# Kernel tuning notes

Hardware: AMD Instinct MI355X
Metric: run time of the kernel (lower is better)

The kernel has to match this reference:

```python
import jax, jax.numpy as jnp
import numpy as np

IN_CH, OUT_CH, SUPPORT = 128, 128, 3
BS, N = 8, 2048


def knn_idx(x, k):
    # x: (bs, n, d) -> (bs, n, k) indices of k nearest (excluding self)
    sq = jnp.sum(x * x, axis=-1)  # (bs, n)
    dist = sq[:, :, None] + sq[:, None, :] - 2.0 * jnp.einsum('bnd,bmd->bnm', x, x)
    _, idx = jax.lax.top_k(-dist, k + 1)  # smallest distances
    return idx[:, :, 1:]


def gather_neighbors(t, idx):
    # t: (bs, n, d), idx: (bs, n, k) -> (bs, n, k, d)
    return jax.vmap(lambda tb, ib: tb[ib])(t, idx)


def l2_normalize(x, axis, eps=1e-12):
    n = jnp.linalg.norm(x, axis=axis, keepdims=True)
    return x / jnp.maximum(n, eps)


def setup_inputs() -> dict:
    key = jax.random.key(0)
    ks = jax.random.split(key, 8)
    stdv = 1.0 / np.sqrt(OUT_CH * (SUPPORT + 1))
    return {
        'vertices': jax.random.normal(ks[0], (BS, N, 3), jnp.float32),
        'feature_map': jax.random.normal(ks[1], (BS, N, IN_CH), jnp.float32),
        'weights': jax.random.uniform(ks[2], (IN_CH, (SUPPORT + 1) * OUT_CH), jnp.float32, -stdv, stdv),
        'bias': jax.random.uniform(ks[3], ((SUPPORT + 1) * OUT_CH,), jnp.float32, -stdv, stdv),
        'directions': jax.random.uniform(ks[4], (3, SUPPORT * OUT_CH), jnp.float32, -stdv, stdv),
        'ste_w': jax.random.normal(ks[5], (OUT_CH, IN_CH), jnp.float32) * (1.0 / np.sqrt(IN_CH)),
        'conv2_w': jax.random.normal(ks[6], (OUT_CH, 2 * OUT_CH), jnp.float32) * (1.0 / np.sqrt(2 * OUT_CH)),
        'neighbor_num': 16,
    }


def reference(vertices, feature_map, weights, bias, directions, ste_w, conv2_w, neighbor_num):
    bs, n, _ = vertices.shape
    k = neighbor_num

    # STE branch: 1x1 conv == per-point linear
    f_ste = jnp.einsum('bnc,oc->bno', feature_map, ste_w)

    # Receptive fields: KNN in feature space ('RF-F'), directions from vertices
    neighbor_index = knn_idx(feature_map, k)                      # (bs, n, k)
    neighbors = gather_neighbors(vertices, neighbor_index)        # (bs, n, k, 3)
    rf_norm = l2_normalize(neighbors - vertices[:, :, None, :], axis=-1)

    # Graph convolution (3D-GCN style)
    sdn = l2_normalize(directions, axis=0)                        # (3, s*out)
    theta = jax.nn.relu(jnp.einsum('bnkd,dm->bnkm', rf_norm, sdn))  # (bs,n,k,s*out)
    fm = feature_map @ weights + bias                             # (bs,n,(s+1)*out)
    feature_center = fm[:, :, :OUT_CH]
    feature_support = gather_neighbors(fm[:, :, OUT_CH:], neighbor_index)  # (bs,n,k,s*out)
    act = (theta * feature_support).reshape(bs, n, k, SUPPORT, OUT_CH)
    act = jnp.max(act, axis=2)          # max over neighbors
    act = jnp.mean(act, axis=2)         # mean over supports
    feature = feature_center + act      # (bs, n, out)

    # ORL: global context via point-space KNN max-pool
    nb_idx2 = knn_idx(vertices, k)
    pooled = jnp.max(gather_neighbors(feature, nb_idx2), axis=2)  # (bs,n,out)
    f_global = jnp.broadcast_to(jnp.mean(pooled, axis=1, keepdims=True), (bs, n, OUT_CH))
    feat_cat = jnp.concatenate([feature, f_global], axis=-1)      # (bs,n,2*out)
    feature_fuse = jnp.einsum('bnc,oc->bno', feat_cat, conv2_w) + feature

    return feature_fuse + f_ste
```

## Files before the change

kernel.cpp:

```cpp
#include <hip/hip_runtime.h>
#include <hip/hip_bf16.h>

#define BS 8
#define NP 2048
#define CIN 128
#define OC 128
#define NSUP 3
#define KNN 16
#define NC 512
#define SC 384
#define CAND 24

typedef __attribute__((ext_vector_type(8))) short bf16x8;
typedef __attribute__((ext_vector_type(4))) float f32x4;

__device__ inline unsigned short f2bf(float x) {
    __hip_bfloat16 h = __float2bfloat16(x);
    return *reinterpret_cast<unsigned short*>(&h);
}
__device__ inline unsigned fkey(float d, int gi) {
    unsigned u = __float_as_uint(d);
    u ^= (unsigned)((int)u >> 31) | 0x80000000u;
    return (u & 0xFFFFF800u) | (unsigned)gi;
}
__device__ inline unsigned umn(unsigned a, unsigned b) { return a < b ? a : b; }
__device__ inline unsigned umx(unsigned a, unsigned b) { return a > b ? a : b; }

__global__ __launch_bounds__(256) void prep_kernel(const float* __restrict__ in,
                                                   float* __restrict__ sq,
                                                   short* __restrict__ outp,
                                                   const float* __restrict__ W,
                                                   const float* __restrict__ conv2,
                                                   const float* __restrict__ stew,
                                                   short* __restrict__ Wt,
                                                   short* __restrict__ conv2b,
                                                   short* __restrict__ stewb) {
    const int tid = threadIdx.x;
    if (blockIdx.x < 1024) {
        const int row = blockIdx.x * 16 + (tid >> 4);
        const int seg = tid & 15;
        const float* p = in + (size_t)row * CIN + seg * 8;
        float4 f0 = *(const float4*)p;
        float4 f1 = *(const float4*)(p + 4);
        bf16x8 s;
        s[0] = (short)f2bf(f0.x); s[1] = (short)f2bf(f0.y);
        s[2] = (short)f2bf(f0.z); s[3] = (short)f2bf(f0.w);
        s[4] = (short)f2bf(f1.x); s[5] = (short)f2bf(f1.y);
        s[6] = (short)f2bf(f1.z); s[7] = (short)f2bf(f1.w);
        *(bf16x8*)&outp[(size_t)row * CIN + seg * 8] = s;
        float ss = f0.x*f0.x + f0.y*f0.y + f0.z*f0.z + f0.w*f0.w
                 + f1.x*f1.x + f1.y*f1.y + f1.z*f1.z + f1.w*f1.w;
#pragma unroll
        for (int msk = 1; msk <= 8; msk <<= 1) ss += __shfl_xor(ss, msk);
        if (seg == 0) sq[row] = ss;
    } else {
        int idx = (blockIdx.x - 1024) * 256 + tid;
        if (idx < NC * CIN) {
            int n = idx >> 7, k = idx & 127;
            Wt[idx] = (short)f2bf(W[(size_t)k * NC + n]);
        } else if (idx < NC * CIN + OC * 2 * OC) {
            int e = idx - NC * CIN;
            conv2b[e] = (short)f2bf(conv2[e]);
        } else {
            int e = idx - NC * CIN - OC * 2 * OC;
            stewb[e] = (short)f2bf(stew[e]);
        }
    }
}

#define TQF 32
#define TPF 64
#define NCHF (NP / TPF)
__global__ __launch_bounds__(256) void knn_feat_kernel(const short* __restrict__ fbb,
                                                       const float* __restrict__ sqn,
                                                       int* __restrict__ cand) {
    __shared__ alignas(16) short Qb[TQF][128];
    __shared__ alignas(16) short Pb[TPF][128];
    __shared__ float sqP[TPF];
    __shared__ unsigned Ds[TQF][68];

    const int b = blockIdx.y, q0 = blockIdx.x * TQF, tid = threadIdx.x;
    const int lane = tid & 63, wid = tid >> 6;
    const short* fb = fbb + (size_t)b * NP * CIN;

    unsigned l0 = 0xFFFFFFFFu, l1 = 0xFFFFFFFFu, l2 = 0xFFFFFFFFu;
    unsigned T = 0xFFFFFFFFu;
    const int gbase = lane & 56;
    const int sub = lane & 7;

    for (int i = 0; i < 2; ++i) {
        int v = i * 256 + tid, row = v >> 4, g = v & 15;
        *(bf16x8*)&Qb[row][(g ^ (row & 7)) * 8] =
            *(const bf16x8*)&fb[(size_t)(q0 + row) * CIN + g * 8];
    }
    for (int i = 0; i < 4; ++i) {
        int v = i * 256 + tid, row = v >> 4, g = v & 15;
        *(bf16x8*)&Pb[row][(g ^ (row & 7)) * 8] =
            *(const bf16x8*)&fb[(size_t)row * CIN + g * 8];
    }
    if (tid < TPF) sqP[tid] = sqn[b * NP + tid];

    const int qt = wid >> 1, ph = wid & 1;
    const int qsl = tid >> 3;
    const int arow = qt * 16 + (lane & 15), asw = arow & 7;
    const int brow0 = ph * 32 + (lane & 15), brow1 = brow0 + 16;
    const int bsw0 = brow0 & 7, bsw1 = brow1 & 7;
    const int oct = lane >> 4;
    const int qrow = qt * 16 + oct * 4;

    for (int ch = 0; ch < NCHF; ++ch) {
        __syncthreads();
        bf16x8 st0, st1, st2, st3;
        float sq_next = 0.f;
        const int nxt = (ch + 1 < NCHF);
        if (nxt) {
            int p0n = (ch + 1) * TPF;
            { int v = tid;       int row = v>>4, g = v&15; st0 = *(const bf16x8*)&fb[(size_t)(p0n+row)*CIN + g*8]; }
            { int v = 256 + tid; int row = v>>4, g = v&15; st1 = *(const bf16x8*)&fb[(size_t)(p0n+row)*CIN + g*8]; }
            { int v = 512 + tid; int row = v>>4, g = v&15; st2 = *(const bf16x8*)&fb[(size_t)(p0n+row)*CIN + g*8]; }
            { int v = 768 + tid; int row = v>>4, g = v&15; st3 = *(const bf16x8*)&fb[(size_t)(p0n+row)*CIN + g*8]; }
            if (tid < TPF) sq_next = sqn[b * NP + p0n + tid];
        }
        f32x4 acc0 = {0.f,0.f,0.f,0.f}, acc1 = {0.f,0.f,0.f,0.f};
#pragma unroll
        for (int kk = 0; kk < 4; ++kk) {
            int g = kk * 4 + oct;
            bf16x8 av  = *(const bf16x8*)&Qb[arow][(g ^ asw) * 8];
            bf16x8 bv0 = *(const bf16x8*)&Pb[brow0][(g ^ bsw0) * 8];
            bf16x8 bv1 = *(const bf16x8*)&Pb[brow1][(g ^ bsw1) * 8];
            acc0 = __builtin_amdgcn_mfma_f32_16x16x32_bf16(av, bv0, acc0, 0, 0, 0);
            acc1 = __builtin_amdgcn_mfma_f32_16x16x32_bf16(av, bv1, acc1, 0, 0, 0);
        }
        const float sp0 = sqP[brow0], sp1 = sqP[brow1];
        const int pg0 = ch * TPF + brow0, pg1 = ch * TPF + brow1;
#pragma unroll
        for (int r = 0; r < 4; ++r) {
            int qg = q0 + qrow + r;
            unsigned k0 = fkey(sp0 - 2.0f * acc0[r], pg0);
            unsigned k1 = fkey(sp1 - 2.0f * acc1[r], pg1);
            if (qg == pg0) k0 = 0xFFFFFFFFu;
            if (qg == pg1) k1 = 0xFFFFFFFFu;
            Ds[qrow + r][brow0] = k0;
            Ds[qrow + r][brow1] = k1;
        }
        __syncthreads();

        {
            uint4 kA = *(const uint4*)&Ds[qsl][sub * 8];
            uint4 kB = *(const uint4*)&Ds[qsl][sub * 8 + 4];
            unsigned kv[8] = {kA.x, kA.y, kA.z, kA.w, kB.x, kB.y, kB.z, kB.w};
#pragma unroll
            for (int j = 0; j < 8; ++j) {
                unsigned long long bal = __ballot(kv[j] < T);
                unsigned gm = (unsigned)(bal >> gbase) & 0xFFu;
                while (gm) {
                    int l = __builtin_ctz(gm);
                    gm &= gm - 1;
                    unsigned k = (unsigned)__shfl((int)kv[j], gbase + l);
                    unsigned pv = (unsigned)__shfl_up((int)l2, 1);
                    if (sub == 0) pv = 0u;
                    unsigned n0 = umn(umx(pv, k), l0);
                    unsigned n1 = umn(umx(l0, k), l1);
                    unsigned n2 = umn(umx(l1, k), l2);
                    l0 = n0; l1 = n1; l2 = n2;
                }
            }
            T = (unsigned)__shfl((int)l2, gbase + 7);
        }
        if (nxt) {
            { int v = tid;       int row = v>>4, g = v&15; *(bf16x8*)&Pb[row][(g^(row&7))*8] = st0; }
            { int v = 256 + tid; int row = v>>4, g = v&15; *(bf16x8*)&Pb[row][(g^(row&7))*8] = st1; }
            { int v = 512 + tid; int row = v>>4, g = v&15; *(bf16x8*)&Pb[row][(g^(row&7))*8] = st2; }
            { int v = 768 + tid; int row = v>>4, g = v&15; *(bf16x8*)&Pb[row][(g^(row&7))*8] = st3; }
            if (tid < TPF) sqP[tid] = sq_next;
        }
    }

    {
        int* dst = cand + ((size_t)b * NP + q0 + qsl) * CAND;
        dst[3 * sub + 0] = (int)(l0 & 0x7FFu);
        dst[3 * sub + 1] = (int)(l1 & 0x7FFu);
        dst[3 * sub + 2] = (int)(l2 & 0x7FFu);
    }
}

__global__ __launch_bounds__(256) void knn_refine_kernel(const float* __restrict__ feat,
                                                         const int* __restrict__ cand,
                                                         int* __restrict__ nbr) {
    __shared__ unsigned long long keyS[4][CAND];
    const int w = threadIdx.x >> 6;
    const int lane = threadIdx.x & 63;
    const int grp = lane >> 4, sl = lane & 15;
    const int gq = blockIdx.x * 4 + w;
    const int b = gq >> 11;
    const int q = gq & (NP - 1);
    const float* fb = feat + (size_t)b * NP * CIN;

    double qd[8];
    {
        float4 a = *(const float4*)&fb[(size_t)q * CIN + sl * 8];
        float4 c = *(const float4*)&fb[(size_t)q * CIN + sl * 8 + 4];
        qd[0] = a.x; qd[1] = a.y; qd[2] = a.z; qd[3] = a.w;
        qd[4] = c.x; qd[5] = c.y; qd[6] = c.z; qd[7] = c.w;
    }
    double sqd = 0.0;
#pragma unroll
    for (int i = 0; i < 8; ++i) sqd += qd[i] * qd[i];
#pragma unroll
    for (int msk = 1; msk <= 8; msk <<= 1) sqd += __shfl_xor(sqd, msk);
    const float sqi = (float)sqd;

    const int* cq = cand + (size_t)gq * CAND;
    int jv[CAND / 4];
#pragma unroll
    for (int t = 0; t < CAND / 4; ++t) jv[t] = cq[t * 4 + grp];

#pragma unroll
    for (int t = 0; t < CAND / 4; ++t) {
        const int j = jv[t];
        float4 a = *(const float4*)&fb[(size_t)j * CIN + sl * 8];
        float4 c = *(const float4*)&fb[(size_t)j * CIN + sl * 8 + 4];
        double fd[8] = {a.x, a.y, a.z, a.w, c.x, c.y, c.z, c.w};
        double dot = 0.0, sj = 0.0;
#pragma unroll
        for (int i = 0; i < 8; ++i) { dot += qd[i] * fd[i]; sj += fd[i] * fd[i]; }
#pragma unroll
        for (int msk = 1; msk <= 8; msk <<= 1) {
            dot += __shfl_xor(dot, msk);
            sj  += __shfl_xor(sj, msk);
        }
        if (sl == 0) {
            float t1 = sqi + (float)sj;
            float t2 = (float)(2.0 * dot);
            float d32 = t1 - t2;
            unsigned u = __float_as_uint(d32);
            u ^= (unsigned)((int)u >> 31) | 0x80000000u;
            keyS[w][t * 4 + grp] = ((unsigned long long)u << 32) | (unsigned)j;
        }
    }
    __syncthreads();
    if (lane < CAND) {
        unsigned long long k = keyS[w][lane];
        int rank = 0;
#pragma unroll
        for (int m = 0; m < CAND; ++m) rank += (keyS[w][m] < k) ? 1 : 0;
        if (rank < KNN) nbr[(size_t)gq * KNN + rank] = (int)(k & 0xFFFFFFFFu);
    }
}

#define TQV 32
__global__ __launch_bounds__(256) void knn_vert_kernel(const float* __restrict__ vert,
                                                       int* __restrict__ nbr) {
    __shared__ alignas(16) float vx[NP], vy[NP], vz[NP];
    const int b = blockIdx.y;
    const int q0 = blockIdx.x * TQV;
    const int tid = threadIdx.x;
    const float* vb = vert + (size_t)b * NP * 3;

    for (int i = 0; i < NP * 3 / 256; ++i) {
        int e = i * 256 + tid;
        float v = vb[e];
        int row = e / 3, comp = e % 3;
        (comp == 0 ? vx : comp == 1 ? vy : vz)[row] = v;
    }
    __syncthreads();

    const int lane = tid & 63;
    const int gbase = lane & 56;
    const int q = tid >> 3;
    const int sub = tid & 7;
    const float qx = vx[q0 + q], qy = vy[q0 + q], qz = vz[q0 + q];

    unsigned l0 = 0xFFFFFFFFu, l1 = 0xFFFFFFFFu, l2 = 0xFFFFFFFFu;
    unsigned T = 0xFFFFFFFFu;

    for (int m = 0; m < NP / 64; ++m) {
        const int p0 = m * 64 + sub * 8;
        float4 xA = *(const float4*)&vx[p0], xB = *(const float4*)&vx[p0 + 4];
        float4 yA = *(const float4*)&vy[p0], yB = *(const float4*)&vy[p0 + 4];
        float4 zA = *(const float4*)&vz[p0], zB = *(const float4*)&vz[p0 + 4];
        float dv[8];
        { float dx = qx-xA.x, dy = qy-yA.x, dz = qz-zA.x; dv[0] = dx*dx+dy*dy+dz*dz; }
        { float dx = qx-xA.y, dy = qy-yA.y, dz = qz-zA.y; dv[1] = dx*dx+dy*dy+dz*dz; }
        { float dx = qx-xA.z, dy = qy-yA.z, dz = qz-zA.z; dv[2] = dx*dx+dy*dy+dz*dz; }
        { float dx = qx-xA.w, dy = qy-yA.w, dz = qz-zA.w; dv[3] = dx*dx+dy*dy+dz*dz; }
        { float dx = qx-xB.x, dy = qy-yB.x, dz = qz-zB.x; dv[4] = dx*dx+dy*dy+dz*dz; }
        { float dx = qx-xB.y, dy = qy-yB.y, dz = qz-zB.y; dv[5] = dx*dx+dy*dy+dz*dz; }
        { float dx = qx-xB.z, dy = qy-yB.z, dz = qz-zB.z; dv[6] = dx*dx+dy*dy+dz*dz; }
        { float dx = qx-xB.w, dy = qy-yB.w, dz = qz-zB.w; dv[7] = dx*dx+dy*dy+dz*dz; }
        unsigned kv[8];
#pragma unroll
        for (int j = 0; j < 8; ++j) kv[j] = fkey(dv[j], p0 + j);
#pragma unroll
        for (int j = 0; j < 8; ++j) {
            unsigned long long bal = __ballot(kv[j] < T);
            unsigned gm = (unsigned)(bal >> gbase) & 0xFFu;
            while (gm) {
                int l = __builtin_ctz(gm);
                gm &= gm - 1;
                unsigned k = (unsigned)__shfl((int)kv[j], gbase + l);
                unsigned pv = (unsigned)__shfl_up((int)l2, 1);
                if (sub == 0) pv = 0u;
                unsigned n0 = umn(umx(pv, k), l0);
                unsigned n1 = umn(umx(l0, k), l1);
                unsigned n2 = umn(umx(l1, k), l2);
                l0 = n0; l1 = n1; l2 = n2;
            }
        }
        T = (unsigned)__shfl((int)l2, gbase + 7);
    }
    {
        int* dst = nbr + ((size_t)b * NP + q0 + q) * KNN;
        unsigned vals[3] = {l0, l1, l2};
#pragma unroll
        for (int e = 0; e < 3; ++e) {
            int r = 3 * sub + e;
            if (r >= 1 && r <= 16) dst[r - 1] = (int)(vals[e] & 0x7FFu);
        }
    }
}

__global__ __launch_bounds__(256) void fm_gemm_kernel(const short* __restrict__ fbb,
                                                      const short* __restrict__ Wt,
                                                      const float* __restrict__ bias,
                                                      float* __restrict__ C) {
    __shared__ alignas(16) short As[64][128];
    const int m0 = blockIdx.x * 64, n0 = blockIdx.y * 128, tid = threadIdx.x;
    const int lane = tid & 63, wid = tid >> 6, oct = lane >> 4;
    for (int i = 0; i < 4; ++i) {
        int v = i * 256 + tid, row = v >> 4, g = v & 15;
        *(bf16x8*)&As[row][(g ^ (row & 7)) * 8] =
            *(const bf16x8*)&fbb[(size_t)(m0 + row) * CIN + g * 8];
    }
    __syncthreads();
    f32x4 acc[4][2] = {};
#pragma unroll
    for (int kk = 0; kk < 4; ++kk) {
        int g = kk * 4 + oct;
        bf16x8 bv[2];
#pragma unroll
        for (int nt = 0; nt < 2; ++nt) {
            int n = n0 + (wid * 2 + nt) * 16 + (lane & 15);
            bv[nt] = *(const bf16x8*)&Wt[(size_t)n * CIN + g * 8];
        }
#pragma unroll
        for (int mt = 0; mt < 4; ++mt) {
            int ar = mt * 16 + (lane & 15);
            bf16x8 av = *(const bf16x8*)&As[ar][(g ^ (ar & 7)) * 8];
#pragma unroll
            for (int nt = 0; nt < 2; ++nt)
                acc[mt][nt] = __builtin_amdgcn_mfma_f32_16x16x32_bf16(av, bv[nt], acc[mt][nt], 0, 0, 0);
        }
    }
#pragma unroll
    for (int mt = 0; mt < 4; ++mt)
#pragma unroll
        for (int nt = 0; nt < 2; ++nt) {
            int n = n0 + (wid * 2 + nt) * 16 + (lane & 15);
            float bsv = bias[n];
            int mbase = m0 + mt * 16 + oct * 4;
#pragma unroll
            for (int r = 0; r < 4; ++r)
                C[(size_t)(mbase + r) * NC + n] = acc[mt][nt][r] + bsv;
        }
}

__global__ __launch_bounds__(128) void act_kernel(const float* __restrict__ fm,
                                                  const int* __restrict__ nbr,
                                                  const float* __restrict__ vert,
                                                  const float* __restrict__ dirs,
                                                  float* __restrict__ feature,
                                                  short* __restrict__ featb) {
    __shared__ int sj[KNN];
    __shared__ float rf[KNN][4];
    const int i = blockIdx.x;
    const int b = blockIdx.y;
    const int tid = threadIdx.x;
    const size_t bi = (size_t)b * NP + i;
    if (tid < KNN) {
        int j = nbr[bi * KNN + tid];
        sj[tid] = j;
        const float* vb = vert + (size_t)b * NP * 3;
        float dx = vb[j * 3 + 0] - vb[i * 3 + 0];
        float dy = vb[j * 3 + 1] - vb[i * 3 + 1];
        float dz = vb[j * 3 + 2] - vb[i * 3 + 2];
        float nrm = sqrtf(dx * dx + dy * dy + dz * dz);
        float den = fmaxf(nrm, 1e-12f);
        rf[tid][0] = dx / den; rf[tid][1] = dy / den; rf[tid][2] = dz / den;
    }
    __syncthreads();
    const int oc = tid;
    float accm = 0.0f;
#pragma unroll
    for (int s = 0; s < NSUP; ++s) {
        int m = s * OC + oc;
        float d0 = dirs[m], d1 = dirs[SC + m], d2 = dirs[2 * SC + m];
        float nrm = sqrtf(d0 * d0 + d1 * d1 + d2 * d2);
        float den = fmaxf(nrm, 1e-12f);
        float s0 = d0 / den, s1 = d1 / den, s2 = d2 / den;
        float vm[4] = {-3.0e38f, -3.0e38f, -3.0e38f, -3.0e38f};
#pragma unroll
        for (int kk = 0; kk < KNN; ++kk) {
            float th = fmaxf(rf[kk][0] * s0 + rf[kk][1] * s1 + rf[kk][2] * s2, 0.0f);
            float sup = fm[((size_t)b * NP + sj[kk]) * NC + OC + m];
            vm[kk & 3] = fmaxf(vm[kk & 3], th * sup);
        }
        accm += fmaxf(fmaxf(vm[0], vm[1]), fmaxf(vm[2], vm[3]));
    }
    float v = fm[bi * NC + oc] + accm / 3.0f;
    feature[bi * OC + oc] = v;
    featb[bi * OC + oc] = (short)f2bf(v);
}

__global__ __launch_bounds__(128) void pool_kernel(const float* __restrict__ feature,
                                                   const int* __restrict__ nbr2,
                                                   float* __restrict__ pooled) {
    __shared__ int sj[KNN];
    const int i = blockIdx.x, b = blockIdx.y, tid = threadIdx.x;
    const size_t bi = (size_t)b * NP + i;
    if (tid < KNN) sj[tid] = nbr2[bi * KNN + tid];
    __syncthreads();
    float m0 = -3.0e38f, m1 = -3.0e38f, m2 = -3.0e38f, m3 = -3.0e38f;
#pragma unroll
    for (int kk = 0; kk < KNN; kk += 4) {
        m0 = fmaxf(m0, feature[((size_t)b * NP + sj[kk + 0]) * OC + tid]);
        m1 = fmaxf(m1, feature[((size_t)b * NP + sj[kk + 1]) * OC + tid]);
        m2 = fmaxf(m2, feature[((size_t)b * NP + sj[kk + 2]) * OC + tid]);
        m3 = fmaxf(m3, feature[((size_t)b * NP + sj[kk + 3]) * OC + tid]);
    }
    pooled[bi * OC + tid] = fmaxf(fmaxf(m0, m1), fmaxf(m2, m3));
}

__global__ __launch_bounds__(128) void partial_kernel(const float* __restrict__ pooled,
                                                      float* __restrict__ part) {
    const int ch = blockIdx.x, b = blockIdx.y, tid = threadIdx.x;
    float s0 = 0.f, s1 = 0.f, s2 = 0.f, s3 = 0.f;
    const float* base = pooled + ((size_t)b * NP + ch * 128) * OC + tid;
    for (int i = 0; i < 128; i += 4) {
        s0 += base[(size_t)(i + 0) * OC];
        s1 += base[(size_t)(i + 1) * OC];
        s2 += base[(size_t)(i + 2) * OC];
        s3 += base[(size_t)(i + 3) * OC];
    }
    part[((size_t)b * 16 + ch) * OC + tid] = ((s0 + s1) + (s2 + s3));
}
__global__ __launch_bounds__(128) void fg_gdot_kernel(const float* __restrict__ part,
                                                      const float* __restrict__ conv2,
                                                      float* __restrict__ gd) {
    __shared__ float fgs[OC];
    const int b = blockIdx.x, tid = threadIdx.x;
    float s = 0.f;
#pragma unroll
    for (int c = 0; c < 16; ++c) s += part[((size_t)b * 16 + c) * OC + tid];
    fgs[tid] = s / (float)NP;
    __syncthreads();
    float g = 0.f;
    const float* w = conv2 + (size_t)tid * 2 * OC + OC;
    for (int c = 0; c < OC; ++c) g += fgs[c] * w[c];
    gd[b * OC + tid] = g;
}

__global__ __launch_bounds__(256) void final_kernel(const short* __restrict__ featb,
                                                    const short* __restrict__ fbb,
                                                    const short* __restrict__ conv2b,
                                                    const short* __restrict__ stewb,
                                                    const float* __restrict__ gd,
                                                    const float* __restrict__ feature,
                                                    float* __restrict__ out) {
    __shared__ alignas(16) short Af[32][128];
    __shared__ alignas(16) short Am[32][128];
    const int m0 = blockIdx.x * 32, tid = threadIdx.x;
    const int lane = tid & 63, wid = tid >> 6, oct = lane >> 4;
    for (int i = 0; i < 2; ++i) {
        int v = i * 256 + tid, row = v >> 4, g = v & 15;
        *(bf16x8*)&Af[row][(g ^ (row & 7)) * 8] =
            *(const bf16x8*)&featb[(size_t)(m0 + row) * OC + g * 8];
        *(bf16x8*)&Am[row][(g ^ (row & 7)) * 8] =
            *(const bf16x8*)&fbb[(size_t)(m0 + row) * CIN + g * 8];
    }
    __syncthreads();
    f32x4 acc[2][2] = {};
#pragma unroll
    for (int kk = 0; kk < 4; ++kk) {
        int g = kk * 4 + oct;
        bf16x8 bC[2], bS[2];
#pragma unroll
        for (int nt = 0; nt < 2; ++nt) {
            int n = (wid * 2 + nt) * 16 + (lane & 15);
            bC[nt] = *(const bf16x8*)&conv2b[(size_t)n * (2 * OC) + g * 8];
            bS[nt] = *(const bf16x8*)&stewb[(size_t)n * CIN + g * 8];
        }
#pragma unroll
        for (int mt = 0; mt < 2; ++mt) {
            int ar = mt * 16 + (lane & 15);
            bf16x8 aF = *(const bf16x8*)&Af[ar][(g ^ (ar & 7)) * 8];
            bf16x8 aM = *(const bf16x8*)&Am[ar][(g ^ (ar & 7)) * 8];
#pragma unroll
            for (int nt = 0; nt < 2; ++nt) {
                acc[mt][nt] = __builtin_amdgcn_mfma_f32_16x16x32_bf16(aF, bC[nt], acc[mt][nt], 0, 0, 0);
                acc[mt][nt] = __builtin_amdgcn_mfma_f32_16x16x32_bf16(aM, bS[nt], acc[mt][nt], 0, 0, 0);
            }
        }
    }
#pragma unroll
    for (int mt = 0; mt < 2; ++mt)
#pragma unroll
        for (int nt = 0; nt < 2; ++nt) {
            int o = (wid * 2 + nt) * 16 + (lane & 15);
            int mbase = m0 + mt * 16 + oct * 4;
#pragma unroll
            for (int r = 0; r < 4; ++r) {
                int m = mbase + r;
                out[(size_t)m * OC + o] = acc[mt][nt][r]
                    + gd[(m >> 11) * OC + o] + feature[(size_t)m * OC + o];
            }
        }
}

extern "C" void kernel_launch(void* const* d_in, const int* in_sizes, int n_in,
                              void* d_out, int out_size, void* d_ws, size_t ws_size,
                              hipStream_t stream) {
    const float* vert  = (const float*)d_in[0];
    const float* fmap  = (const float*)d_in[1];
    const float* W     = (const float*)d_in[2];
    const float* bias  = (const float*)d_in[3];
    const float* dirs  = (const float*)d_in[4];
    const float* stew  = (const float*)d_in[5];
    const float* conv2 = (const float*)d_in[6];
    float* out = (float*)d_out;

    float* ws      = (float*)d_ws;
    float* sqn     = ws;
    short* fbb     = (short*)(sqn + 16384);
    float* C1      = sqn + 16384 + 1048576;
    float* feature = C1 + 8388608;
    short* featb   = (short*)(feature + 2097152);
    float* gd      = feature + 2097152 + 1048576;
    short* Wt      = (short*)(gd + 1024);
    short* conv2b  = Wt + 65536;
    short* stewb   = conv2b + 32768;
    int*   nbr1    = (int*)(stewb + 16384);
    int*   nbr2    = nbr1 + 262144;
    float* part    = (float*)(nbr2 + 262144);
    int*   cand    = (int*)C1;
    float* pooled  = C1;

    prep_kernel<<<1472, 256, 0, stream>>>(fmap, sqn, fbb, W, conv2, stew, Wt, conv2b, stewb);
    knn_feat_kernel<<<dim3(64, 8), 256, 0, stream>>>(fbb, sqn, cand);
    knn_refine_kernel<<<4096, 256, 0, stream>>>(fmap, cand, nbr1);
    knn_vert_kernel<<<dim3(64, 8), 256, 0, stream>>>(vert, nbr2);
    fm_gemm_kernel<<<dim3(256, 4), 256, 0, stream>>>(fbb, Wt, bias, C1);
    act_kernel<<<dim3(2048, 8), 128, 0, stream>>>(C1, nbr1, vert, dirs, feature, featb);
    pool_kernel<<<dim3(2048, 8), 128, 0, stream>>>(feature, nbr2, pooled);
    partial_kernel<<<dim3(16, 8), 128, 0, stream>>>(pooled, part);
    fg_gdot_kernel<<<8, 128, 0, stream>>>(part, conv2, gd);
    final_kernel<<<512, 256, 0, stream>>>(featb, fbb, conv2b, stewb, gd, feature, out);
}
```

Before: 227.8 us.

## Split feature KNN scan across two blocks per query tile, refine 48 candidates

```diff
diff --git a/kernel.cpp b/kernel.cpp
--- a/kernel.cpp
+++ b/kernel.cpp
@@ -10,6 +10,7 @@
 #define NC 512
 #define SC 384
 #define CAND 24
+#define CANDR 48
 
 typedef __attribute__((ext_vector_type(8))) short bf16x8;
 typedef __attribute__((ext_vector_type(4))) float f32x4;
@@ -70,7 +71,7 @@
 
 #define TQF 32
 #define TPF 64
-#define NCHF (NP / TPF)
+#define NCHH 16
 __global__ __launch_bounds__(256) void knn_feat_kernel(const short* __restrict__ fbb,
                                                        const float* __restrict__ sqn,
                                                        int* __restrict__ cand) {
@@ -79,7 +80,10 @@
     __shared__ float sqP[TPF];
     __shared__ unsigned Ds[TQF][68];
 
-    const int b = blockIdx.y, q0 = blockIdx.x * TQF, tid = threadIdx.x;
+    const int b = blockIdx.y, tid = threadIdx.x;
+    const int hx = blockIdx.x & 1;
+    const int q0 = (blockIdx.x >> 1) * TQF;
+    const int pbase = hx * (NP / 2);
     const int lane = tid & 63, wid = tid >> 6;
     const short* fb = fbb + (size_t)b * NP * CIN;
 
@@ -96,9 +100,9 @@
     for (int i = 0; i < 4; ++i) {
         int v = i * 256 + tid, row = v >> 4, g = v & 15;
         *(bf16x8*)&Pb[row][(g ^ (row & 7)) * 8] =
-            *(const bf16x8*)&fb[(size_t)row * CIN + g * 8];
-    }
-    if (tid < TPF) sqP[tid] = sqn[b * NP + tid];
+            *(const bf16x8*)&fb[(size_t)(pbase + row) * CIN + g * 8];
+    }
+    if (tid < TPF) sqP[tid] = sqn[b * NP + pbase + tid];
 
     const int qt = wid >> 1, ph = wid & 1;
     const int qsl = tid >> 3;
@@ -108,13 +112,13 @@
     const int oct = lane >> 4;
     const int qrow = qt * 16 + oct * 4;
 
-    for (int ch = 0; ch < NCHF; ++ch) {
+    for (int ch = 0; ch < NCHH; ++ch) {
         __syncthreads();
         bf16x8 st0, st1, st2, st3;
         float sq_next = 0.f;
-        const int nxt = (ch + 1 < NCHF);
+        const int nxt = (ch + 1 < NCHH);
         if (nxt) {
-            int p0n = (ch + 1) * TPF;
+            int p0n = pbase + (ch + 1) * TPF;
             { int v = tid;       int row = v>>4, g = v&15; st0 = *(const bf16x8*)&fb[(size_t)(p0n+row)*CIN + g*8]; }
             { int v = 256 + tid; int row = v>>4, g = v&15; st1 = *(const bf16x8*)&fb[(size_t)(p0n+row)*CIN + g*8]; }
             { int v = 512 + tid; int row = v>>4, g = v&15; st2 = *(const bf16x8*)&fb[(size_t)(p0n+row)*CIN + g*8]; }
@@ -132,7 +136,7 @@
             acc1 = __builtin_amdgcn_mfma_f32_16x16x32_bf16(av, bv1, acc1, 0, 0, 0);
         }
         const float sp0 = sqP[brow0], sp1 = sqP[brow1];
-        const int pg0 = ch * TPF + brow0, pg1 = ch * TPF + brow1;
+        const int pg0 = pbase + ch * TPF + brow0, pg1 = pbase + ch * TPF + brow1;
 #pragma unroll
         for (int r = 0; r < 4; ++r) {
             int qg = q0 + qrow + r;
@@ -177,7 +181,7 @@
     }
 
     {
-        int* dst = cand + ((size_t)b * NP + q0 + qsl) * CAND;
+        int* dst = cand + ((size_t)b * NP + q0 + qsl) * CANDR + hx * CAND;
         dst[3 * sub + 0] = (int)(l0 & 0x7FFu);
         dst[3 * sub + 1] = (int)(l1 & 0x7FFu);
         dst[3 * sub + 2] = (int)(l2 & 0x7FFu);
@@ -187,7 +191,7 @@
 __global__ __launch_bounds__(256) void knn_refine_kernel(const float* __restrict__ feat,
                                                          const int* __restrict__ cand,
                                                          int* __restrict__ nbr) {
-    __shared__ unsigned long long keyS[4][CAND];
+    __shared__ unsigned long long keyS[4][CANDR];
     const int w = threadIdx.x >> 6;
     const int lane = threadIdx.x & 63;
     const int grp = lane >> 4, sl = lane & 15;
@@ -210,13 +214,13 @@
     for (int msk = 1; msk <= 8; msk <<= 1) sqd += __shfl_xor(sqd, msk);
     const float sqi = (float)sqd;
 
-    const int* cq = cand + (size_t)gq * CAND;
-    int jv[CAND / 4];
-#pragma unroll
-    for (int t = 0; t < CAND / 4; ++t) jv[t] = cq[t * 4 + grp];
-
-#pragma unroll
-    for (int t = 0; t < CAND / 4; ++t) {
+    const int* cq = cand + (size_t)gq * CANDR;
+    int jv[CANDR / 4];
+#pragma unroll
+    for (int t = 0; t < CANDR / 4; ++t) jv[t] = cq[t * 4 + grp];
+
+#pragma unroll
+    for (int t = 0; t < CANDR / 4; ++t) {
         const int j = jv[t];
         float4 a = *(const float4*)&fb[(size_t)j * CIN + sl * 8];
         float4 c = *(const float4*)&fb[(size_t)j * CIN + sl * 8 + 4];
@@ -239,11 +243,11 @@
         }
     }
     __syncthreads();
-    if (lane < CAND) {
+    if (lane < CANDR) {
         unsigned long long k = keyS[w][lane];
         int rank = 0;
 #pragma unroll
-        for (int m = 0; m < CAND; ++m) rank += (keyS[w][m] < k) ? 1 : 0;
+        for (int m = 0; m < CANDR; ++m) rank += (keyS[w][m] < k) ? 1 : 0;
         if (rank < KNN) nbr[(size_t)gq * KNN + rank] = (int)(k & 0xFFFFFFFFu);
     }
 }
@@ -546,7 +550,7 @@
     float* pooled  = C1;
 
     prep_kernel<<<1472, 256, 0, stream>>>(fmap, sqn, fbb, W, conv2, stew, Wt, conv2b, stewb);
-    knn_feat_kernel<<<dim3(64, 8), 256, 0, stream>>>(fbb, sqn, cand);
+    knn_feat_kernel<<<dim3(128, 8), 256, 0, stream>>>(fbb, sqn, cand);
     knn_refine_kernel<<<4096, 256, 0, stream>>>(fmap, cand, nbr1);
     knn_vert_kernel<<<dim3(64, 8), 256, 0, stream>>>(vert, nbr2);
     fm_gemm_kernel<<<dim3(256, 4), 256, 0, stream>>>(fbb, Wt, bias, C1);
```

After: 242.9 us. 1.07x slower.
